# Kernel tuning notes

Measured on AMD Instinct MI355X. Metric: run time of the kernel, lower is better.

The kernel has to match this reference:

```python
import jax, jax.numpy as jnp
import numpy as np

D_MODEL = 1024
NUM_HEADS = 16
HEAD_DIM = D_MODEL // NUM_HEADS
B, T_Q, T_KV = 4, 4096, 4096


def setup_inputs() -> dict:
    key = jax.random.key(0)
    ks = jax.random.split(key, 10)
    s_in = 1.0 / np.sqrt(D_MODEL)
    s_out = 1.0 / np.sqrt(D_MODEL)
    return {
        "q": jax.random.normal(ks[0], (B, T_Q, D_MODEL), jnp.float32),
        "kv": jax.random.normal(ks[1], (B, T_KV, D_MODEL), jnp.float32),
        # per-head projection weights stacked: [H, d_model, head_dim]
        "Wq": jax.random.uniform(ks[2], (NUM_HEADS, D_MODEL, HEAD_DIM), jnp.float32, -s_in, s_in),
        "bq": jax.random.uniform(ks[3], (NUM_HEADS, HEAD_DIM), jnp.float32, -s_in, s_in),
        "Wk": jax.random.uniform(ks[4], (NUM_HEADS, D_MODEL, HEAD_DIM), jnp.float32, -s_in, s_in),
        "bk": jax.random.uniform(ks[5], (NUM_HEADS, HEAD_DIM), jnp.float32, -s_in, s_in),
        "Wv": jax.random.uniform(ks[6], (NUM_HEADS, D_MODEL, HEAD_DIM), jnp.float32, -s_in, s_in),
        "bv": jax.random.uniform(ks[7], (NUM_HEADS, HEAD_DIM), jnp.float32, -s_in, s_in),
        "Wo": jax.random.uniform(ks[8], (D_MODEL, D_MODEL), jnp.float32, -s_out, s_out),
        "bo": jax.random.uniform(ks[9], (D_MODEL,), jnp.float32, -s_out, s_out),
    }


def reference(q, kv, Wq, bq, Wk, bk, Wv, bv, Wo, bo):
    Bsz, Tq, _ = q.shape
    # per-head projections fused into one batched GEMM each: [b,t,d] x [h,d,e] -> [b,h,t,e]
    qh = jnp.einsum('btd,hde->bhte', q, Wq) + bq[None, :, None, :]
    kh = jnp.einsum('btd,hde->bhte', kv, Wk) + bk[None, :, None, :]
    vh = jnp.einsum('btd,hde->bhte', kv, Wv) + bv[None, :, None, :]
    # squared feature map
    qh = qh * qh
    kh = kh * kh
    # O(N) linear attention aggregation
    kv_sum = jnp.einsum('bhnd,bhne->bhde', kh, vh)           # [B,H,e,e]
    z = 1.0 / (jnp.einsum('bhnd,bhd->bhn', qh, kh.sum(axis=2)) + 1e-6)  # [B,H,Tq]
    attn = jnp.einsum('bhnd,bhde,bhn->bhne', qh, kv_sum, z)  # [B,H,Tq,e]
    attn = attn.transpose(0, 2, 1, 3).reshape(Bsz, Tq, D_MODEL)
    return attn @ Wo.T + bo
```

## Files before the change

kernel.cpp:

```cpp
#include <hip/hip_runtime.h>

#define BSZ 4
#define TSEQ 4096
#define DM 1024
#define NH 16
#define HD 64
#define BT (BSZ * TSEQ)
#define INV_LOSCALE (1.0f / 4096.0f)

using f32x4 = __attribute__((ext_vector_type(4))) float;
using f16x8 = __attribute__((ext_vector_type(8))) _Float16;
using u32x2 = __attribute__((ext_vector_type(2))) unsigned;
using u32x4 = __attribute__((ext_vector_type(4))) unsigned;

typedef const __attribute__((address_space(1))) void* gas_ptr;
typedef __attribute__((address_space(3))) void* las_ptr;

__device__ __forceinline__ void gload16(const void* g, void* l) {
    __builtin_amdgcn_global_load_lds((gas_ptr)g, (las_ptr)l, 16, 0, 0);
}

__device__ __forceinline__ void split1(float x, _Float16& h, _Float16& l) {
    h = (_Float16)x;
    l = (_Float16)((x - (float)h) * 4096.0f);
}
__device__ __forceinline__ unsigned pack2(_Float16 a, _Float16 b) {
    return (unsigned)__builtin_bit_cast(unsigned short, a) |
           ((unsigned)__builtin_bit_cast(unsigned short, b) << 16);
}
__device__ __forceinline__ f32x4 mfma_f16(f16x8 a, f16x8 b, f32x4 c) {
    return __builtin_amdgcn_mfma_f32_16x16x32_f16(a, b, c, 0, 0, 0);
}

__global__ __launch_bounds__(256) void fragsplit_kernel(const float* __restrict__ in,
        _Float16* __restrict__ hi, _Float16* __restrict__ lo) {
    const int C = blockIdx.x * 256 + threadIdx.x;
    const int l15 = C & 15, quad = (C >> 4) & 3, rb = (C >> 6) & 3;
    const int s = (C >> 8) & 31, panel = C >> 13;
    const size_t src = ((size_t)(panel * 64 + rb * 16 + l15)) * DM + s * 32 + quad * 8;
    f32x4 v0 = *(const f32x4*)&in[src];
    f32x4 v1 = *(const f32x4*)&in[src + 4];
    _Float16 h[8], l[8];
    #pragma unroll
    for (int j = 0; j < 4; ++j) { split1(v0[j], h[j], l[j]); split1(v1[j], h[4 + j], l[4 + j]); }
    ((u32x4*)hi)[C] = (u32x4){pack2(h[0],h[1]), pack2(h[2],h[3]), pack2(h[4],h[5]), pack2(h[6],h[7])};
    ((u32x4*)lo)[C] = (u32x4){pack2(l[0],l[1]), pack2(l[2],l[3]), pack2(l[4],l[5]), pack2(l[6],l[7])};
}

__global__ __launch_bounds__(256) void wsplit_kernel(
    const float* __restrict__ Wq, const float* __restrict__ Wk, const float* __restrict__ Wv,
    _Float16* __restrict__ qh, _Float16* __restrict__ ql,
    _Float16* __restrict__ kh, _Float16* __restrict__ kl,
    _Float16* __restrict__ vh, _Float16* __restrict__ vl) {
    const int tid = threadIdx.x;
    const int k0 = blockIdx.x * 64, h = blockIdx.y, w = blockIdx.z;
    const float* __restrict__ W = (w == 0) ? Wq : (w == 1) ? Wk : Wv;
    _Float16* __restrict__ dh = (w == 0) ? qh : (w == 1) ? kh : vh;
    _Float16* __restrict__ dl = (w == 0) ? ql : (w == 1) ? kl : vl;
    __shared__ __align__(16) float ws_[64][68];
    #pragma unroll
    for (int it = 0; it < 4; ++it) {
        int idx = it * 256 + tid;
        int r = idx >> 4, c4 = (idx & 15) * 4;
        *(f32x4*)&ws_[r][c4] = *(const f32x4*)&W[((size_t)h * DM + k0 + r) * HD + c4];
    }
    __syncthreads();
    const int n = tid >> 2, kq16 = (tid & 3) * 16;
    _Float16 hh[16], ll[16];
    #pragma unroll
    for (int j = 0; j < 16; ++j) split1(ws_[kq16 + j][n], hh[j], ll[j]);
    #pragma unroll
    for (int c = 0; c < 2; ++c) {
        int kg = k0 + kq16 + c * 8;
        int s = kg >> 5, quad = (kg >> 3) & 3;
        size_t chunk = (size_t)(h * 32 + s) * 256 + ((n >> 4) * 4 + quad) * 16 + (n & 15);
        ((u32x4*)dh)[chunk] = (u32x4){pack2(hh[c*8+0],hh[c*8+1]), pack2(hh[c*8+2],hh[c*8+3]),
                                      pack2(hh[c*8+4],hh[c*8+5]), pack2(hh[c*8+6],hh[c*8+7])};
        ((u32x4*)dl)[chunk] = (u32x4){pack2(ll[c*8+0],ll[c*8+1]), pack2(ll[c*8+2],ll[c*8+3]),
                                      pack2(ll[c*8+4],ll[c*8+5]), pack2(ll[c*8+6],ll[c*8+7])};
    }
}

__global__ __launch_bounds__(256, 2) void kv_stats_kernel(
    const _Float16* __restrict__ kv_hi, const _Float16* __restrict__ kv_lo,
    const _Float16* __restrict__ wkt_hi, const _Float16* __restrict__ wkt_lo,
    const _Float16* __restrict__ wvt_hi, const _Float16* __restrict__ wvt_lo,
    const float* __restrict__ bk, const float* __restrict__ bv,
    float* __restrict__ kv_sum, float* __restrict__ ksum)
{
    const int tid = threadIdx.x;
    const int lane = tid & 63, wave = tid >> 6, quad = lane >> 4, l15 = lane & 15;
    const int b = blockIdx.z, h = blockIdx.y, bx = blockIdx.x;

    __shared__ __align__(16) char smem[65536];
    float* khs = (float*)smem;
    float* vhs = (float*)(smem + 32768);

    const int isV = wave >> 1, half = wave & 1;
    const size_t btile = (size_t)h * 32;
    const int ty = tid >> 4, tx = tid & 15;

    f32x4 akv[4] = {};
    float aks[4] = {0.f, 0.f, 0.f, 0.f};

    for (int sub = 0; sub < 2; ++sub) {
        const size_t apan = (size_t)(b * 64 + bx * 4 + sub * 2);
        auto stage = [&](int p, int s) {
            char* dst = smem + p * 32768 + tid * 16;
            const size_t a0 = (apan * 32 + s) * 2048 + tid * 8;
            const size_t a1 = ((apan + 1) * 32 + s) * 2048 + tid * 8;
            const size_t bo = (btile + s) * 2048 + tid * 8;
            gload16(&kv_hi[a0], dst);
            gload16(&kv_hi[a1], dst + 4096);
            gload16(&kv_lo[a0], dst + 8192);
            gload16(&kv_lo[a1], dst + 12288);
            gload16(&wkt_hi[bo], dst + 16384);
            gload16(&wkt_lo[bo], dst + 20480);
            gload16(&wvt_hi[bo], dst + 24576);
            gload16(&wvt_lo[bo], dst + 28672);
        };

        f32x4 acc_h[4][4] = {}, acc_c[4][4] = {};
        stage(0, 0);
        for (int s = 0; s < 32; ++s) {
            const int p = s & 1;
            if (s < 31) {
                stage(p ^ 1, s + 1);
                asm volatile("s_waitcnt vmcnt(8)" ::: "memory");
            } else {
                asm volatile("s_waitcnt vmcnt(0)" ::: "memory");
            }
            __builtin_amdgcn_s_barrier();
            __builtin_amdgcn_sched_barrier(0);
            const char* bufc = smem + p * 32768;
            const _Float16* a_hi = (const _Float16*)bufc;
            const _Float16* a_lo = (const _Float16*)(bufc + 8192);
            const _Float16* bh = (const _Float16*)(bufc + (isV ? 24576 : 16384));
            const _Float16* bl = (const _Float16*)(bufc + (isV ? 28672 : 20480));
            f16x8 afh[4], afl[4], bfh[4], bfl[4];
            #pragma unroll
            for (int mt = 0; mt < 4; ++mt) {
                afh[mt] = *(const f16x8*)&a_hi[half * 2048 + mt * 512 + lane * 8];
                afl[mt] = *(const f16x8*)&a_lo[half * 2048 + mt * 512 + lane * 8];
            }
            #pragma unroll
            for (int nt = 0; nt < 4; ++nt) {
                bfh[nt] = *(const f16x8*)&bh[nt * 512 + lane * 8];
                bfl[nt] = *(const f16x8*)&bl[nt * 512 + lane * 8];
            }
            #pragma unroll
            for (int mt = 0; mt < 4; ++mt)
                #pragma unroll
                for (int nt = 0; nt < 4; ++nt) {
                    acc_h[mt][nt] = mfma_f16(afh[mt], bfh[nt], acc_h[mt][nt]);
                    acc_c[mt][nt] = mfma_f16(afh[mt], bfl[nt], acc_c[mt][nt]);
                    acc_c[mt][nt] = mfma_f16(afl[mt], bfh[nt], acc_c[mt][nt]);
                }
            __builtin_amdgcn_s_barrier();
            __builtin_amdgcn_sched_barrier(0);
        }

        {
            const float* __restrict__ bias = (isV ? bv : bk) + h * HD;
            float* __restrict__ outs = isV ? vhs : khs;
            float bia[4];
            #pragma unroll
            for (int nt = 0; nt < 4; ++nt) bia[nt] = bias[nt * 16 + l15];
            #pragma unroll
            for (int mt = 0; mt < 4; ++mt)
                #pragma unroll
                for (int nt = 0; nt < 4; ++nt)
                    #pragma unroll
                    for (int r = 0; r < 4; ++r) {
                        int t = half * 64 + mt * 16 + quad * 4 + r;
                        float v = acc_h[mt][nt][r] + INV_LOSCALE * acc_c[mt][nt][r] + bia[nt];
                        if (!isV) v = v * v;
                        outs[t * 64 + nt * 16 + l15] = v;
                    }
        }
        __syncthreads();

        #pragma unroll 4
        for (int t = 0; t < 128; ++t) {
            f32x4 kd = *(const f32x4*)&khs[t * 64 + ty * 4];
            f32x4 ve = *(const f32x4*)&vhs[t * 64 + tx * 4];
            #pragma unroll
            for (int i = 0; i < 4; ++i) {
                aks[i] += kd[i];
                akv[i] += kd[i] * ve;
            }
        }
        __syncthreads();
    }

    float* kvp = kv_sum + (size_t)(b * NH + h) * HD * HD;
    #pragma unroll
    for (int i = 0; i < 4; ++i)
        #pragma unroll
        for (int j = 0; j < 4; ++j)
            atomicAdd(&kvp[(ty * 4 + i) * HD + tx * 4 + j], akv[i][j]);
    if (tx == 0) {
        float* ksp = ksum + (b * NH + h) * HD;
        #pragma unroll
        for (int i = 0; i < 4; ++i) atomicAdd(&ksp[ty * 4 + i], aks[i]);
    }
}

__global__ __launch_bounds__(256, 3) void q_attn_ps_kernel(
    const _Float16* __restrict__ qf_hi, const _Float16* __restrict__ qf_lo,
    const _Float16* __restrict__ wqt_hi, const _Float16* __restrict__ wqt_lo,
    const float* __restrict__ bq,
    const float* __restrict__ kv_sum, const float* __restrict__ ksum,
    _Float16* __restrict__ attn_hi, _Float16* __restrict__ attn_lo)
{
    const int tid = threadIdx.x;
    const int lane = tid & 63, wave = tid >> 6, quad = lane >> 4, l15 = lane & 15;
    const int b = blockIdx.z, h = blockIdx.y, bx = blockIdx.x;

    __shared__ __align__(16) char smem[51200];
    __shared__ float z_s[128], ks_s[64];

    if (tid < 64) ks_s[tid] = ksum[(b * NH + h) * HD + tid];

    const size_t apan = (size_t)(b * 64 + bx * 2);
    const size_t btile = (size_t)h * 32;

    auto stage = [&](int p, int s) {
        char* dst = smem + p * 24576 + tid * 16;
        const size_t a0 = (apan * 32 + s) * 2048 + tid * 8;
        const size_t a1 = ((apan + 1) * 32 + s) * 2048 + tid * 8;
        const size_t bo = (btile + s) * 2048 + tid * 8;
        gload16(&qf_hi[a0], dst);
        gload16(&qf_hi[a1], dst + 4096);
        gload16(&qf_lo[a0], dst + 8192);
        gload16(&qf_lo[a1], dst + 12288);
        gload16(&wqt_hi[bo], dst + 16384);
        gload16(&wqt_lo[bo], dst + 20480);
    };

    f32x4 acc_h[2][4] = {}, acc_c[2][4] = {};
    stage(0, 0);
    for (int s = 0; s < 32; ++s) {
        const int p = s & 1;
        if (s < 31) {
            stage(p ^ 1, s + 1);
            asm volatile("s_waitcnt vmcnt(6)" ::: "memory");
        } else {
            asm volatile("s_waitcnt vmcnt(0)" ::: "memory");
        }
        __builtin_amdgcn_s_barrier();
        __builtin_amdgcn_sched_barrier(0);
        const char* bufc = smem + p * 24576;
        const _Float16* a_hi = (const _Float16*)bufc;
        const _Float16* a_lo = (const _Float16*)(bufc + 8192);
        f16x8 afh[2], afl[2], bfh[4], bfl[4];
        #pragma unroll
        for (int mt = 0; mt < 2; ++mt) {
            int fo = (wave * 2 + mt) * 512 + lane * 8;
            afh[mt] = *(const f16x8*)&a_hi[fo];
            afl[mt] = *(const f16x8*)&a_lo[fo];
        }
        #pragma unroll
        for (int nt = 0; nt < 4; ++nt) {
            bfh[nt] = *(const f16x8*)((const _Float16*)(bufc + 16384) + nt * 512 + lane * 8);
            bfl[nt] = *(const f16x8*)((const _Float16*)(bufc + 20480) + nt * 512 + lane * 8);
        }
        #pragma unroll
        for (int mt = 0; mt < 2; ++mt)
            #pragma unroll
            for (int nt = 0; nt < 4; ++nt) {
                acc_h[mt][nt] = mfma_f16(afh[mt], bfh[nt], acc_h[mt][nt]);
                acc_c[mt][nt] = mfma_f16(afh[mt], bfl[nt], acc_c[mt][nt]);
                acc_c[mt][nt] = mfma_f16(afl[mt], bfh[nt], acc_c[mt][nt]);
            }
        __builtin_amdgcn_s_barrier();
        __builtin_amdgcn_sched_barrier(0);
    }

    float* qs = (float*)smem;
    {
        const float* __restrict__ bias = bq + h * HD;
        float zp[2][4] = {};
        #pragma unroll
        for (int nt = 0; nt < 4; ++nt) {
            int d = nt * 16 + l15;
            float bia = bias[d];
            float ks  = ks_s[d];
            #pragma unroll
            for (int mt = 0; mt < 2; ++mt)
                #pragma unroll
                for (int r = 0; r < 4; ++r) {
                    int t = wave * 32 + mt * 16 + quad * 4 + r;
                    float v = acc_h[mt][nt][r] + INV_LOSCALE * acc_c[mt][nt][r] + bia;
                    float v2 = v * v;
                    qs[t * 68 + d] = v2;
                    zp[mt][r] = fmaf(v2, ks, zp[mt][r]);
                }
        }
        #pragma unroll
        for (int mt = 0; mt < 2; ++mt)
            #pragma unroll
            for (int r = 0; r < 4; ++r) {
                float p = zp[mt][r];
                p += __shfl_xor(p, 1);
                p += __shfl_xor(p, 2);
                p += __shfl_xor(p, 4);
                p += __shfl_xor(p, 8);
                if (l15 == 0) z_s[wave * 32 + mt * 16 + quad * 4 + r] = 1.f / (p + 1e-6f);
            }
    }
    __syncthreads();

    float* kvs = (float*)(smem + 34816);
    {
        const float* __restrict__ kvp = kv_sum + (size_t)(b * NH + h) * HD * HD;
        #pragma unroll
        for (int it = 0; it < 4; ++it) {
            int idx = it * 256 + tid;
            int r = idx >> 4, c = (idx & 15) * 4;
            *(f32x4*)&kvs[r * 64 + c] = *(const f32x4*)&kvp[r * HD + c];
        }
    }
    __syncthreads();

    const int ty = tid >> 4, tx = tid & 15;
    f32x4 sv[8] = {};
    #pragma unroll 4
    for (int d = 0; d < 64; d += 4) {
        f32x4 b0 = *(const f32x4*)&kvs[(d + 0) * 64 + tx * 4];
        f32x4 b1 = *(const f32x4*)&kvs[(d + 1) * 64 + tx * 4];
        f32x4 b2 = *(const f32x4*)&kvs[(d + 2) * 64 + tx * 4];
        f32x4 b3 = *(const f32x4*)&kvs[(d + 3) * 64 + tx * 4];
        #pragma unroll
        for (int i = 0; i < 8; ++i) {
            f32x4 av = *(const f32x4*)&qs[(ty * 8 + i) * 68 + d];
            sv[i] += av.x * b0 + av.y * b1 + av.z * b2 + av.w * b3;
        }
    }
    const int s_out = h * 2 + (tx >> 3);
    const int kq = (tx >> 1) & 3;
    const int rem8 = (tx & 1) * 8;
    #pragma unroll
    for (int i = 0; i < 8; ++i) {
        int t = ty * 8 + i;
        const size_t opanel = (size_t)b * 64 + bx * 2 + (t >> 6);
        const int tt = t & 63;
        f32x4 o = sv[i] * z_s[t];
        _Float16 hh[4], ll[4];
        #pragma unroll
        for (int j = 0; j < 4; ++j) split1(o[j], hh[j], ll[j]);
        size_t cb = (((opanel * 32 + s_out) * 256 + ((tt >> 4) * 4 + kq) * 16 + (tt & 15)) << 4) + rem8;
        *(u32x2*)((char*)attn_hi + cb) = (u32x2){pack2(hh[0], hh[1]), pack2(hh[2], hh[3])};
        *(u32x2*)((char*)attn_lo + cb) = (u32x2){pack2(ll[0], ll[1]), pack2(ll[2], ll[3])};
    }
}

__global__ __launch_bounds__(256, 3) void q_attn_kernel(
    const float* __restrict__ q,
    const _Float16* __restrict__ wqt_hi, const _Float16* __restrict__ wqt_lo,
    const float* __restrict__ bq,
    const float* __restrict__ kv_sum, const float* __restrict__ ksum,
    _Float16* __restrict__ attn_hi, _Float16* __restrict__ attn_lo)
{
    const int tid = threadIdx.x;
    const int lane = tid & 63, wave = tid >> 6, quad = lane >> 4, l15 = lane & 15;
    const int b = blockIdx.z, h = blockIdx.y, bx = blockIdx.x;
    const int t0 = bx * 64;

    __shared__ __align__(16) char smem[32768];
    __shared__ __align__(16) float qs[64 * 68];
    __shared__ float z_s[64], ks_s[64];

    if (tid < 64) ks_s[tid] = ksum[(b * NH + h) * HD + tid];

    const int arb = tid >> 6, aquad = (tid >> 4) & 3, al15 = tid & 15;
    const float* __restrict__ qrow =
        q + ((size_t)b * TSEQ + t0 + arb * 16 + al15) * DM + aquad * 8;
    const size_t btile = (size_t)h * 32;

    auto asplit_write = [&](int p, f32x4 v0, f32x4 v1) {
        _Float16 hh[8], ll[8];
        #pragma unroll
        for (int j = 0; j < 4; ++j) { split1(v0[j], hh[j], ll[j]); split1(v1[j], hh[4+j], ll[4+j]); }
        char* dst = smem + p * 16384 + tid * 16;
        *(u32x4*)dst =
            (u32x4){pack2(hh[0],hh[1]), pack2(hh[2],hh[3]), pack2(hh[4],hh[5]), pack2(hh[6],hh[7])};
        *(u32x4*)(dst + 4096) =
            (u32x4){pack2(ll[0],ll[1]), pack2(ll[2],ll[3]), pack2(ll[4],ll[5]), pack2(ll[6],ll[7])};
    };
    auto stageB = [&](int p, int s) {
        char* dst = smem + p * 16384 + 8192 + tid * 16;
        const size_t bo = (btile + s) * 2048 + tid * 8;
        gload16(&wqt_hi[bo], dst);
        gload16(&wqt_lo[bo], dst + 4096);
    };

    f32x4 acc_h[4] = {}, acc_c[4] = {};
    f32x4 v0 = *(const f32x4*)&qrow[0];
    f32x4 v1 = *(const f32x4*)&qrow[4];
    asplit_write(0, v0, v1);
    stageB(0, 0);
    v0 = *(const f32x4*)&qrow[32];
    v1 = *(const f32x4*)&qrow[36];
    asm volatile("s_waitcnt vmcnt(2) lgkmcnt(0)" ::: "memory");
    __builtin_amdgcn_s_barrier();
    __builtin_amdgcn_sched_barrier(0);

    for (int s = 0; s < 32; ++s) {
        const int p = s & 1;
        if (s < 31) {
            stageB(p ^ 1, s + 1);
            asplit_write(p ^ 1, v0, v1);
            if (s < 30) {
                v0 = *(const f32x4*)&qrow[(s + 2) * 32];
                v1 = *(const f32x4*)&qrow[(s + 2) * 32 + 4];
            }
            asm volatile("s_waitcnt vmcnt(4) lgkmcnt(0)" ::: "memory");
        } else {
            asm volatile("s_waitcnt vmcnt(0)" ::: "memory");
        }
        __builtin_amdgcn_s_barrier();
        __builtin_amdgcn_sched_barrier(0);
        const char* bufc = smem + p * 16384;
        f16x8 afh = *(const f16x8*)((const _Float16*)bufc + wave * 512 + lane * 8);
        f16x8 afl = *(const f16x8*)((const _Float16*)(bufc + 4096) + wave * 512 + lane * 8);
        f16x8 bfh[4], bfl[4];
        #pragma unroll
        for (int nt = 0; nt < 4; ++nt) {
            bfh[nt] = *(const f16x8*)((const _Float16*)(bufc + 8192) + nt * 512 + lane * 8);
            bfl[nt] = *(const f16x8*)((const _Float16*)(bufc + 12288) + nt * 512 + lane * 8);
        }
        #pragma unroll
        for (int nt = 0; nt < 4; ++nt) {
            acc_h[nt] = mfma_f16(afh, bfh[nt], acc_h[nt]);
            acc_c[nt] = mfma_f16(afh, bfl[nt], acc_c[nt]);
            acc_c[nt] = mfma_f16(afl, bfh[nt], acc_c[nt]);
        }
        __builtin_amdgcn_s_barrier();
        __builtin_amdgcn_sched_barrier(0);
    }

    {
        const int mrow0 = wave * 16;
        const float* __restrict__ bias = bq + h * HD;
        float zp[4] = {0.f, 0.f, 0.f, 0.f};
        #pragma unroll
        for (int nt = 0; nt < 4; ++nt) {
            int d = nt * 16 + l15;
            float bia = bias[d];
            float ks  = ks_s[d];
            #pragma unroll
            for (int r = 0; r < 4; ++r) {
                int t = mrow0 + quad * 4 + r;
                float v = acc_h[nt][r] + INV_LOSCALE * acc_c[nt][r] + bia;
                float v2 = v * v;
                qs[t * 68 + d] = v2;
                zp[r] = fmaf(v2, ks, zp[r]);
            }
        }
        #pragma unroll
        for (int r = 0; r < 4; ++r) {
            float p = zp[r];
            p += __shfl_xor(p, 1);
            p += __shfl_xor(p, 2);
            p += __shfl_xor(p, 4);
            p += __shfl_xor(p, 8);
            if (l15 == 0) z_s[mrow0 + quad * 4 + r] = 1.f / (p + 1e-6f);
        }
    }
    __syncthreads();

    float* kvs = (float*)smem;
    {
        const float* __restrict__ kvp = kv_sum + (size_t)(b * NH + h) * HD * HD;
        #pragma unroll
        for (int it = 0; it < 4; ++it) {
            int idx = it * 256 + tid;
            int r = idx >> 4, c = (idx & 15) * 4;
            *(f32x4*)&kvs[r * 64 + c] = *(const f32x4*)&kvp[r * HD + c];
        }
    }
    __syncthreads();

    const int ty = tid >> 4, tx = tid & 15;
    f32x4 sv[4] = {};
    #pragma unroll 4
    for (int d = 0; d < 64; d += 4) {
        f32x4 b0 = *(const f32x4*)&kvs[(d + 0) * 64 + tx * 4];
        f32x4 b1 = *(const f32x4*)&kvs[(d + 1) * 64 + tx * 4];
        f32x4 b2 = *(const f32x4*)&kvs[(d + 2) * 64 + tx * 4];
        f32x4 b3 = *(const f32x4*)&kvs[(d + 3) * 64 + tx * 4];
        #pragma unroll
        for (int i = 0; i < 4; ++i) {
            f32x4 av = *(const f32x4*)&qs[(ty * 4 + i) * 68 + d];
            sv[i] += av.x * b0 + av.y * b1 + av.z * b2 + av.w * b3;
        }
    }
    const size_t opanel = (size_t)b * 64 + bx;
    const int s_out = h * 2 + (tx >> 3);
    const int kq = (tx >> 1) & 3;
    const int rem8 = (tx & 1) * 8;
    #pragma unroll
    for (int i = 0; i < 4; ++i) {
        int t = ty * 4 + i;
        f32x4 o = sv[i] * z_s[t];
        _Float16 hh[4], ll[4];
        #pragma unroll
        for (int j = 0; j < 4; ++j) split1(o[j], hh[j], ll[j]);
        size_t cb = (((opanel * 32 + s_out) * 256 + ((t >> 4) * 4 + kq) * 16 + (t & 15)) << 4) + rem8;
        *(u32x2*)((char*)attn_hi + cb) = (u32x2){pack2(hh[0], hh[1]), pack2(hh[2], hh[3])};
        *(u32x2*)((char*)attn_lo + cb) = (u32x2){pack2(ll[0], ll[1]), pack2(ll[2], ll[3])};
    }
}

__global__ __launch_bounds__(256, 3) void out_proj_kernel(
    const _Float16* __restrict__ attn_hi, const _Float16* __restrict__ attn_lo,
    const _Float16* __restrict__ wo_hi, const _Float16* __restrict__ wo_lo,
    const float* __restrict__ bo, float* __restrict__ out)
{
    const int tid = threadIdx.x;
    const int lane = tid & 63, wave = tid >> 6, quad = lane >> 4, l15 = lane & 15;
    const int n0 = blockIdx.x * 64;
    const size_t m0 = (size_t)blockIdx.y * 128;

    __shared__ __align__(16) char smem[49152];
    float* cs = (float*)smem;

    const size_t ap0 = (m0 >> 6) * 32, ap1 = ap0 + 32;
    const size_t bpn = (size_t)(n0 >> 6) * 32;

    auto stage = [&](int p, int s) {
        char* dst = smem + p * 24576 + tid * 16;
        const size_t co = (size_t)s * 2048 + tid * 8;
        gload16(&attn_hi[ap0 * 2048 + co], dst);
        gload16(&attn_hi[ap1 * 2048 + co], dst + 4096);
        gload16(&attn_lo[ap0 * 2048 + co], dst + 8192);
        gload16(&attn_lo[ap1 * 2048 + co], dst + 12288);
        gload16(&wo_hi[bpn * 2048 + co],  dst + 16384);
        gload16(&wo_lo[bpn * 2048 + co],  dst + 20480);
    };

    const int panel = wave >> 1;
    f32x4 acc_h[2][4] = {}, acc_c[2][4] = {};
    stage(0, 0);
    for (int s = 0; s < 32; ++s) {
        const int p = s & 1;
        if (s < 31) {
            stage(p ^ 1, s + 1);
            asm volatile("s_waitcnt vmcnt(6)" ::: "memory");
        } else {
            asm volatile("s_waitcnt vmcnt(0)" ::: "memory");
        }
        __builtin_amdgcn_s_barrier();
        __builtin_amdgcn_sched_barrier(0);
        const char* bufc = smem + p * 24576;
        f16x8 afh[2], afl[2], bfh[4], bfl[4];
        #pragma unroll
        for (int mt = 0; mt < 2; ++mt) {
            int rbl = (wave & 1) * 2 + mt;
            afh[mt] = *(const f16x8*)((const _Float16*)(bufc + panel * 4096) + rbl * 512 + lane * 8);
            afl[mt] = *(const f16x8*)((const _Float16*)(bufc + 8192 + panel * 4096) + rbl * 512 + lane * 8);
        }
        #pragma unroll
        for (int nt = 0; nt < 4; ++nt) {
            bfh[nt] = *(const f16x8*)((const _Float16*)(bufc + 16384) + nt * 512 + lane * 8);
            bfl[nt] = *(const f16x8*)((const _Float16*)(bufc + 20480) + nt * 512 + lane * 8);
        }
        #pragma unroll
        for (int mt = 0; mt < 2; ++mt)
            #pragma unroll
            for (int nt = 0; nt < 4; ++nt) {
                acc_h[mt][nt] = mfma_f16(afh[mt], bfh[nt], acc_h[mt][nt]);
                acc_c[mt][nt] = mfma_f16(afh[mt], bfl[nt], acc_c[mt][nt]);
                acc_c[mt][nt] = mfma_f16(afl[mt], bfh[nt], acc_c[mt][nt]);
            }
        __builtin_amdgcn_s_barrier();
        __builtin_amdgcn_sched_barrier(0);
    }

    {
        float bia[4];
        #pragma unroll
        for (int nt = 0; nt < 4; ++nt) bia[nt] = bo[n0 + nt * 16 + l15];
        #pragma unroll
        for (int mt = 0; mt < 2; ++mt)
            #pragma unroll
            for (int nt = 0; nt < 4; ++nt)
                #pragma unroll
                for (int r = 0; r < 4; ++r) {
                    int t = wave * 32 + mt * 16 + quad * 4 + r;
                    cs[t * 64 + nt * 16 + l15] =
                        acc_h[mt][nt][r] + INV_LOSCALE * acc_c[mt][nt][r] + bia[nt];
                }
    }
    __syncthreads();
    #pragma unroll
    for (int it = 0; it < 8; ++it) {
        int idx = it * 256 + tid;
        int r = idx >> 4, c = (idx & 15) * 4;
        *(f32x4*)&out[(m0 + r) * DM + n0 + c] = *(f32x4*)&cs[r * 64 + c];
    }
}

extern "C" void kernel_launch(void* const* d_in, const int* in_sizes, int n_in,
                              void* d_out, int out_size, void* d_ws, size_t ws_size,
                              hipStream_t stream) {
    const float* q  = (const float*)d_in[0];
    const float* kv = (const float*)d_in[1];
    const float* Wq = (const float*)d_in[2];
    const float* bq = (const float*)d_in[3];
    const float* Wk = (const float*)d_in[4];
    const float* bk = (const float*)d_in[5];
    const float* Wv = (const float*)d_in[6];
    const float* bv = (const float*)d_in[7];
    const float* Wo = (const float*)d_in[8];
    const float* bo = (const float*)d_in[9];
    float* out = (float*)d_out;

    char* p = (char*)d_ws;
    float* kv_sum = (float*)p;              p += (size_t)BSZ * NH * HD * HD * 4;
    float* ksum   = (float*)p;              p += (size_t)BSZ * NH * HD * 4;
    _Float16* wqt_hi = (_Float16*)p;        p += (size_t)NH * HD * DM * 2;
    _Float16* wqt_lo = (_Float16*)p;        p += (size_t)NH * HD * DM * 2;
    _Float16* wkt_hi = (_Float16*)p;        p += (size_t)NH * HD * DM * 2;
    _Float16* wkt_lo = (_Float16*)p;        p += (size_t)NH * HD * DM * 2;
    _Float16* wvt_hi = (_Float16*)p;        p += (size_t)NH * HD * DM * 2;
    _Float16* wvt_lo = (_Float16*)p;        p += (size_t)NH * HD * DM * 2;
    _Float16* wo_hi  = (_Float16*)p;        p += (size_t)DM * DM * 2;
    _Float16* wo_lo  = (_Float16*)p;        p += (size_t)DM * DM * 2;
    _Float16* buf_hi = (_Float16*)p;        p += (size_t)BT * DM * 2;
    _Float16* buf_lo = (_Float16*)p;        p += (size_t)BT * DM * 2;
    _Float16* qf_hi  = (_Float16*)p;        p += (size_t)BT * DM * 2;
    _Float16* qf_lo  = (_Float16*)p;        p += (size_t)BT * DM * 2;
    const bool big = ws_size >= (size_t)(p - (char*)d_ws);

    size_t zero_bytes = ((size_t)BSZ * NH * HD * HD + (size_t)BSZ * NH * HD) * sizeof(float);
    hipMemsetAsync(d_ws, 0, zero_bytes, stream);

    fragsplit_kernel<<<(BT * DM / 8) / 256, 256, 0, stream>>>(kv, buf_hi, buf_lo);
    wsplit_kernel<<<dim3(DM / 64, NH, 3), 256, 0, stream>>>(
        Wq, Wk, Wv, wqt_hi, wqt_lo, wkt_hi, wkt_lo, wvt_hi, wvt_lo);
    fragsplit_kernel<<<(DM * DM / 8) / 256, 256, 0, stream>>>(Wo, wo_hi, wo_lo);

    kv_stats_kernel<<<dim3(TSEQ / 256, NH, BSZ), 256, 0, stream>>>(
        buf_hi, buf_lo, wkt_hi, wkt_lo, wvt_hi, wvt_lo, bk, bv, kv_sum, ksum);

    if (big) {
        fragsplit_kernel<<<(BT * DM / 8) / 256, 256, 0, stream>>>(q, qf_hi, qf_lo);
        q_attn_ps_kernel<<<dim3(TSEQ / 128, NH, BSZ), 256, 0, stream>>>(
            qf_hi, qf_lo, wqt_hi, wqt_lo, bq, kv_sum, ksum, buf_hi, buf_lo);
    } else {
        q_attn_kernel<<<dim3(TSEQ / 64, NH, BSZ), 256, 0, stream>>>(
            q, wqt_hi, wqt_lo, bq, kv_sum, ksum, buf_hi, buf_lo);
    }
    out_proj_kernel<<<dim3(DM / 64, BT / 128), 256, 0, stream>>>(
        buf_hi, buf_lo, wo_hi, wo_lo, bo, out);
}
```

Measured before the change: 650.5 us.

## Fold kv_sum into Wo per batch and use MFMA for KV statistics

Measured after the change: 626.0 us. 3.8% less time.

```diff
diff --git a/kernel.cpp b/kernel.cpp
--- a/kernel.cpp
+++ b/kernel.cpp
@@ -93,15 +93,18 @@
     const int b = blockIdx.z, h = blockIdx.y, bx = blockIdx.x;
 
     __shared__ __align__(16) char smem[65536];
-    float* khs = (float*)smem;
-    float* vhs = (float*)(smem + 32768);
+    _Float16* khT_h = (_Float16*)smem;
+    _Float16* khT_l = (_Float16*)(smem + 16384);
+    _Float16* vhT_h = (_Float16*)(smem + 32768);
+    _Float16* vhT_l = (_Float16*)(smem + 49152);
 
     const int isV = wave >> 1, half = wave & 1;
     const size_t btile = (size_t)h * 32;
-    const int ty = tid >> 4, tx = tid & 15;
-
-    f32x4 akv[4] = {};
-    float aks[4] = {0.f, 0.f, 0.f, 0.f};
+
+    f32x4 racc_h[4] = {}, racc_c[4] = {};
+    f32x4 rk_h = {}, rk_c = {};
+    const f16x8 ones = __builtin_bit_cast(f16x8,
+        (u32x4){0x3C003C00u, 0x3C003C00u, 0x3C003C00u, 0x3C003C00u});
 
     for (int sub = 0; sub < 2; ++sub) {
         const size_t apan = (size_t)(b * 64 + bx * 4 + sub * 2);
@@ -162,32 +165,46 @@
 
         {
             const float* __restrict__ bias = (isV ? bv : bk) + h * HD;
-            float* __restrict__ outs = isV ? vhs : khs;
+            _Float16* __restrict__ dh = isV ? vhT_h : khT_h;
+            _Float16* __restrict__ dl = isV ? vhT_l : khT_l;
             float bia[4];
             #pragma unroll
             for (int nt = 0; nt < 4; ++nt) bia[nt] = bias[nt * 16 + l15];
             #pragma unroll
-            for (int mt = 0; mt < 4; ++mt)
+            for (int mt = 0; mt < 4; ++mt) {
+                const int S = half * 2 + (mt >> 1);
+                const int tq = (mt & 1) * 2 + (quad >> 1);
+                const int eo = (quad & 1) * 4;
                 #pragma unroll
-                for (int nt = 0; nt < 4; ++nt)
+                for (int nt = 0; nt < 4; ++nt) {
+                    _Float16 hh[4], ll[4];
                     #pragma unroll
                     for (int r = 0; r < 4; ++r) {
-                        int t = half * 64 + mt * 16 + quad * 4 + r;
                         float v = acc_h[mt][nt][r] + INV_LOSCALE * acc_c[mt][nt][r] + bia[nt];
                         if (!isV) v = v * v;
-                        outs[t * 64 + nt * 16 + l15] = v;
+                        split1(v, hh[r], ll[r]);
                     }
+                    int fo = S * 2048 + (nt * 4 + tq) * 128 + l15 * 8 + eo;
+                    *(u32x2*)&dh[fo] = (u32x2){pack2(hh[0], hh[1]), pack2(hh[2], hh[3])};
+                    *(u32x2*)&dl[fo] = (u32x2){pack2(ll[0], ll[1]), pack2(ll[2], ll[3])};
+                }
+            }
         }
         __syncthreads();
 
-        #pragma unroll 4
-        for (int t = 0; t < 128; ++t) {
-            f32x4 kd = *(const f32x4*)&khs[t * 64 + ty * 4];
-            f32x4 ve = *(const f32x4*)&vhs[t * 64 + tx * 4];
-            #pragma unroll
-            for (int i = 0; i < 4; ++i) {
-                aks[i] += kd[i];
-                akv[i] += kd[i] * ve;
+        #pragma unroll
+        for (int S = 0; S < 4; ++S) {
+            f16x8 ah = *(const f16x8*)&khT_h[S * 2048 + wave * 512 + lane * 8];
+            f16x8 al = *(const f16x8*)&khT_l[S * 2048 + wave * 512 + lane * 8];
+            rk_h = mfma_f16(ah, ones, rk_h);
+            rk_c = mfma_f16(al, ones, rk_c);
+            #pragma unroll
+            for (int nt = 0; nt < 4; ++nt) {
+                f16x8 bh = *(const f16x8*)&vhT_h[S * 2048 + nt * 512 + lane * 8];
+                f16x8 bl = *(const f16x8*)&vhT_l[S * 2048 + nt * 512 + lane * 8];
+                racc_h[nt] = mfma_f16(ah, bh, racc_h[nt]);
+                racc_c[nt] = mfma_f16(ah, bl, racc_c[nt]);
+                racc_c[nt] = mfma_f16(al, bh, racc_c[nt]);
             }
         }
         __syncthreads();
@@ -195,29 +212,76 @@
 
     float* kvp = kv_sum + (size_t)(b * NH + h) * HD * HD;
     #pragma unroll
-    for (int i = 0; i < 4; ++i)
-        #pragma unroll
-        for (int j = 0; j < 4; ++j)
-            atomicAdd(&kvp[(ty * 4 + i) * HD + tx * 4 + j], akv[i][j]);
-    if (tx == 0) {
+    for (int nt = 0; nt < 4; ++nt)
+        #pragma unroll
+        for (int r = 0; r < 4; ++r)
+            atomicAdd(&kvp[(wave * 16 + quad * 4 + r) * HD + nt * 16 + l15],
+                      racc_h[nt][r] + INV_LOSCALE * racc_c[nt][r]);
+    if (l15 == 0) {
         float* ksp = ksum + (b * NH + h) * HD;
         #pragma unroll
-        for (int i = 0; i < 4; ++i) atomicAdd(&ksp[ty * 4 + i], aks[i]);
+        for (int r = 0; r < 4; ++r)
+            atomicAdd(&ksp[wave * 16 + quad * 4 + r], rk_h[r] + INV_LOSCALE * rk_c[r]);
+    }
+}
+
+__global__ __launch_bounds__(256) void pmat_kernel(
+    const float* __restrict__ kv_sum, const float* __restrict__ Wo,
+    _Float16* __restrict__ pt_hi, _Float16* __restrict__ pt_lo)
+{
+    const int tid = threadIdx.x;
+    const int opan = blockIdx.x, h = blockIdx.y, b = blockIdx.z;
+    __shared__ __align__(16) float kvsT[64][68];
+    __shared__ __align__(16) float wos[64][68];
+    const float* __restrict__ kvp = kv_sum + (size_t)(b * NH + h) * HD * HD;
+    #pragma unroll
+    for (int it = 0; it < 4; ++it) {
+        int idx = it * 256 + tid;
+        int d = idx >> 4, e4 = (idx & 15) * 4;
+        f32x4 v = *(const f32x4*)&kvp[d * HD + e4];
+        kvsT[e4 + 0][d] = v.x; kvsT[e4 + 1][d] = v.y;
+        kvsT[e4 + 2][d] = v.z; kvsT[e4 + 3][d] = v.w;
+        int o = idx >> 4;
+        *(f32x4*)&wos[o][e4] = *(const f32x4*)&Wo[(size_t)(opan * 64 + o) * DM + h * HD + e4];
+    }
+    __syncthreads();
+    const int ty = tid >> 4, tx = tid & 15;
+    f32x4 sv[4] = {};
+    #pragma unroll 8
+    for (int e = 0; e < 64; ++e) {
+        f32x4 kv4 = *(const f32x4*)&kvsT[e][tx * 4];
+        #pragma unroll
+        for (int i = 0; i < 4; ++i) sv[i] += wos[ty * 4 + i][e] * kv4;
+    }
+    const int d0 = tx * 4;
+    const int S = h * 2 + (d0 >> 5);
+    const int kq = (d0 >> 3) & 3;
+    const int rem8 = (d0 & 4) ? 8 : 0;
+    #pragma unroll
+    for (int i = 0; i < 4; ++i) {
+        int ol = ty * 4 + i;
+        f32x4 o4 = sv[i] * INV_LOSCALE;
+        _Float16 hh[4], ll[4];
+        #pragma unroll
+        for (int j = 0; j < 4; ++j) split1(o4[j], hh[j], ll[j]);
+        size_t cb = ((((size_t)(b * 16 + opan) * 32 + S) * 256 +
+                      ((ol >> 4) * 4 + kq) * 16 + (ol & 15)) << 4) + rem8;
+        *(u32x2*)((char*)pt_hi + cb) = (u32x2){pack2(hh[0], hh[1]), pack2(hh[2], hh[3])};
+        *(u32x2*)((char*)pt_lo + cb) = (u32x2){pack2(ll[0], ll[1]), pack2(ll[2], ll[3])};
     }
 }
 
 __global__ __launch_bounds__(256, 3) void q_attn_ps_kernel(
     const _Float16* __restrict__ qf_hi, const _Float16* __restrict__ qf_lo,
     const _Float16* __restrict__ wqt_hi, const _Float16* __restrict__ wqt_lo,
-    const float* __restrict__ bq,
-    const float* __restrict__ kv_sum, const float* __restrict__ ksum,
+    const float* __restrict__ bq, const float* __restrict__ ksum,
     _Float16* __restrict__ attn_hi, _Float16* __restrict__ attn_lo)
 {
     const int tid = threadIdx.x;
     const int lane = tid & 63, wave = tid >> 6, quad = lane >> 4, l15 = lane & 15;
     const int b = blockIdx.z, h = blockIdx.y, bx = blockIdx.x;
 
-    __shared__ __align__(16) char smem[51200];
+    __shared__ __align__(16) char smem[49152];
     __shared__ float z_s[128], ks_s[64];
 
     if (tid < 64) ks_s[tid] = ksum[(b * NH + h) * HD + tid];
@@ -306,52 +370,31 @@
                 p += __shfl_xor(p, 2);
                 p += __shfl_xor(p, 4);
                 p += __shfl_xor(p, 8);
-                if (l15 == 0) z_s[wave * 32 + mt * 16 + quad * 4 + r] = 1.f / (p + 1e-6f);
+                if (l15 == 0) z_s[wave * 32 + mt * 16 + quad * 4 + r] = 4096.0f / (p + 1e-6f);
             }
     }
     __syncthreads();
 
-    float* kvs = (float*)(smem + 34816);
-    {
-        const float* __restrict__ kvp = kv_sum + (size_t)(b * NH + h) * HD * HD;
-        #pragma unroll
-        for (int it = 0; it < 4; ++it) {
-            int idx = it * 256 + tid;
-            int r = idx >> 4, c = (idx & 15) * 4;
-            *(f32x4*)&kvs[r * 64 + c] = *(const f32x4*)&kvp[r * HD + c];
-        }
-    }
-    __syncthreads();
-
-    const int ty = tid >> 4, tx = tid & 15;
-    f32x4 sv[8] = {};
-    #pragma unroll 4
-    for (int d = 0; d < 64; d += 4) {
-        f32x4 b0 = *(const f32x4*)&kvs[(d + 0) * 64 + tx * 4];
-        f32x4 b1 = *(const f32x4*)&kvs[(d + 1) * 64 + tx * 4];
-        f32x4 b2 = *(const f32x4*)&kvs[(d + 2) * 64 + tx * 4];
-        f32x4 b3 = *(const f32x4*)&kvs[(d + 3) * 64 + tx * 4];
-        #pragma unroll
-        for (int i = 0; i < 8; ++i) {
-            f32x4 av = *(const f32x4*)&qs[(ty * 8 + i) * 68 + d];
-            sv[i] += av.x * b0 + av.y * b1 + av.z * b2 + av.w * b3;
-        }
-    }
-    const int s_out = h * 2 + (tx >> 3);
-    const int kq = (tx >> 1) & 3;
-    const int rem8 = (tx & 1) * 8;
-    #pragma unroll
-    for (int i = 0; i < 8; ++i) {
-        int t = ty * 8 + i;
-        const size_t opanel = (size_t)b * 64 + bx * 2 + (t >> 6);
-        const int tt = t & 63;
-        f32x4 o = sv[i] * z_s[t];
-        _Float16 hh[4], ll[4];
-        #pragma unroll
-        for (int j = 0; j < 4; ++j) split1(o[j], hh[j], ll[j]);
-        size_t cb = (((opanel * 32 + s_out) * 256 + ((tt >> 4) * 4 + kq) * 16 + (tt & 15)) << 4) + rem8;
-        *(u32x2*)((char*)attn_hi + cb) = (u32x2){pack2(hh[0], hh[1]), pack2(hh[2], hh[3])};
-        *(u32x2*)((char*)attn_lo + cb) = (u32x2){pack2(ll[0], ll[1]), pack2(ll[2], ll[3])};
+    #pragma unroll
+    for (int it = 0; it < 4; ++it) {
+        int cid = it * 256 + tid;
+        int lp = cid >> 9, Sl = (cid >> 8) & 1, c = cid & 255;
+        int t = lp * 64 + (c >> 6) * 16 + (c & 15);
+        int d = Sl * 32 + ((c >> 4) & 3) * 8;
+        f32x4 a0 = *(const f32x4*)&qs[t * 68 + d];
+        f32x4 a1 = *(const f32x4*)&qs[t * 68 + d + 4];
+        float z = z_s[t];
+        _Float16 hh[8], ll[8];
+        #pragma unroll
+        for (int j = 0; j < 4; ++j) {
+            split1(z * a0[j], hh[j], ll[j]);
+            split1(z * a1[j], hh[4 + j], ll[4 + j]);
+        }
+        size_t cb = (((size_t)(b * 64 + bx * 2 + lp) * 32 + h * 2 + Sl) * 256 + c) << 4;
+        *(u32x4*)((char*)attn_hi + cb) =
+            (u32x4){pack2(hh[0],hh[1]), pack2(hh[2],hh[3]), pack2(hh[4],hh[5]), pack2(hh[6],hh[7])};
+        *(u32x4*)((char*)attn_lo + cb) =
+            (u32x4){pack2(ll[0],ll[1]), pack2(ll[2],ll[3]), pack2(ll[4],ll[5]), pack2(ll[6],ll[7])};
     }
 }
 
@@ -513,6 +556,98 @@
     }
 }
 
+__global__ __launch_bounds__(256, 3) void out_proj_p_kernel(
+    const _Float16* __restrict__ attn_hi, const _Float16* __restrict__ attn_lo,
+    const _Float16* __restrict__ pt_hi, const _Float16* __restrict__ pt_lo,
+    const float* __restrict__ bo, float* __restrict__ out)
+{
+    const int tid = threadIdx.x;
+    const int lane = tid & 63, wave = tid >> 6, quad = lane >> 4, l15 = lane & 15;
+    const int n0 = blockIdx.x * 64;
+    const size_t m0 = (size_t)blockIdx.y * 128;
+
+    __shared__ __align__(16) char smem[49152];
+    float* cs = (float*)smem;
+
+    const size_t ap0 = (m0 >> 6) * 32, ap1 = ap0 + 32;
+    const int bb = (int)(m0 >> 12);
+    const _Float16* __restrict__ pbh = pt_hi + (size_t)bb * 16 * 32 * 2048;
+    const _Float16* __restrict__ pbl = pt_lo + (size_t)bb * 16 * 32 * 2048;
+    const size_t bpn = (size_t)(n0 >> 6) * 32;
+
+    auto stage = [&](int p, int s) {
+        char* dst = smem + p * 24576 + tid * 16;
+        const size_t co = (size_t)s * 2048 + tid * 8;
+        gload16(&attn_hi[ap0 * 2048 + co], dst);
+        gload16(&attn_hi[ap1 * 2048 + co], dst + 4096);
+        gload16(&attn_lo[ap0 * 2048 + co], dst + 8192);
+        gload16(&attn_lo[ap1 * 2048 + co], dst + 12288);
+        gload16(&pbh[(bpn + s) * 2048 + tid * 8], dst + 16384);
+        gload16(&pbl[(bpn + s) * 2048 + tid * 8], dst + 20480);
+    };
+
+    const int panel = wave >> 1;
+    f32x4 acc_h[2][4] = {}, acc_c[2][4] = {};
+    stage(0, 0);
+    for (int s = 0; s < 32; ++s) {
+        const int p = s & 1;
+        if (s < 31) {
+            stage(p ^ 1, s + 1);
+            asm volatile("s_waitcnt vmcnt(6)" ::: "memory");
+        } else {
+            asm volatile("s_waitcnt vmcnt(0)" ::: "memory");
+        }
+        __builtin_amdgcn_s_barrier();
+        __builtin_amdgcn_sched_barrier(0);
+        const char* bufc = smem + p * 24576;
+        f16x8 afh[2], afl[2], bfh[4], bfl[4];
+        #pragma unroll
+        for (int mt = 0; mt < 2; ++mt) {
+            int rbl = (wave & 1) * 2 + mt;
+            afh[mt] = *(const f16x8*)((const _Float16*)(bufc + panel * 4096) + rbl * 512 + lane * 8);
+            afl[mt] = *(const f16x8*)((const _Float16*)(bufc + 8192 + panel * 4096) + rbl * 512 + lane * 8);
+        }
+        #pragma unroll
+        for (int nt = 0; nt < 4; ++nt) {
+            bfh[nt] = *(const f16x8*)((const _Float16*)(bufc + 16384) + nt * 512 + lane * 8);
+            bfl[nt] = *(const f16x8*)((const _Float16*)(bufc + 20480) + nt * 512 + lane * 8);
+        }
+        #pragma unroll
+        for (int mt = 0; mt < 2; ++mt)
+            #pragma unroll
+            for (int nt = 0; nt < 4; ++nt) {
+                acc_h[mt][nt] = mfma_f16(afh[mt], bfh[nt], acc_h[mt][nt]);
+                acc_c[mt][nt] = mfma_f16(afh[mt], bfl[nt], acc_c[mt][nt]);
+                acc_c[mt][nt] = mfma_f16(afl[mt], bfh[nt], acc_c[mt][nt]);
+            }
+        __builtin_amdgcn_s_barrier();
+        __builtin_amdgcn_sched_barrier(0);
+    }
+
+    {
+        float bia[4];
+        #pragma unroll
+        for (int nt = 0; nt < 4; ++nt) bia[nt] = bo[n0 + nt * 16 + l15];
+        #pragma unroll
+        for (int mt = 0; mt < 2; ++mt)
+            #pragma unroll
+            for (int nt = 0; nt < 4; ++nt)
+                #pragma unroll
+                for (int r = 0; r < 4; ++r) {
+                    int t = wave * 32 + mt * 16 + quad * 4 + r;
+                    cs[t * 64 + nt * 16 + l15] =
+                        acc_h[mt][nt][r] + INV_LOSCALE * acc_c[mt][nt][r] + bia[nt];
+                }
+    }
+    __syncthreads();
+    #pragma unroll
+    for (int it = 0; it < 8; ++it) {
+        int idx = it * 256 + tid;
+        int r = idx >> 4, c = (idx & 15) * 4;
+        *(f32x4*)&out[(m0 + r) * DM + n0 + c] = *(f32x4*)&cs[r * 64 + c];
+    }
+}
+
 __global__ __launch_bounds__(256, 3) void out_proj_kernel(
     const _Float16* __restrict__ attn_hi, const _Float16* __restrict__ attn_lo,
     const _Float16* __restrict__ wo_hi, const _Float16* __restrict__ wo_lo,
@@ -536,8 +671,8 @@
         gload16(&attn_hi[ap1 * 2048 + co], dst + 4096);
         gload16(&attn_lo[ap0 * 2048 + co], dst + 8192);
         gload16(&attn_lo[ap1 * 2048 + co], dst + 12288);
-        gload16(&wo_hi[bpn * 2048 + co],  dst + 16384);
-        gload16(&wo_lo[bpn * 2048 + co],  dst + 20480);
+        gload16(&wo_hi[(bpn + s) * 2048 + tid * 8], dst + 16384);
+        gload16(&wo_lo[(bpn + s) * 2048 + tid * 8], dst + 20480);
     };
 
     const int panel = wave >> 1;
@@ -632,6 +767,8 @@
     _Float16* buf_lo = (_Float16*)p;        p += (size_t)BT * DM * 2;
     _Float16* qf_hi  = (_Float16*)p;        p += (size_t)BT * DM * 2;
     _Float16* qf_lo  = (_Float16*)p;        p += (size_t)BT * DM * 2;
+    _Float16* pt_hi  = (_Float16*)p;        p += (size_t)BSZ * DM * DM * 2;
+    _Float16* pt_lo  = (_Float16*)p;        p += (size_t)BSZ * DM * DM * 2;
     const bool big = ws_size >= (size_t)(p - (char*)d_ws);
 
     size_t zero_bytes = ((size_t)BSZ * NH * HD * HD + (size_t)BSZ * NH * HD) * sizeof(float);
@@ -640,19 +777,23 @@
     fragsplit_kernel<<<(BT * DM / 8) / 256, 256, 0, stream>>>(kv, buf_hi, buf_lo);
     wsplit_kernel<<<dim3(DM / 64, NH, 3), 256, 0, stream>>>(
         Wq, Wk, Wv, wqt_hi, wqt_lo, wkt_hi, wkt_lo, wvt_hi, wvt_lo);
-    fragsplit_kernel<<<(DM * DM / 8) / 256, 256, 0, stream>>>(Wo, wo_hi, wo_lo);
+    if (!big)
+        fragsplit_kernel<<<(DM * DM / 8) / 256, 256, 0, stream>>>(Wo, wo_hi, wo_lo);
 
     kv_stats_kernel<<<dim3(TSEQ / 256, NH, BSZ), 256, 0, stream>>>(
         buf_hi, buf_lo, wkt_hi, wkt_lo, wvt_hi, wvt_lo, bk, bv, kv_sum, ksum);
 
     if (big) {
         fragsplit_kernel<<<(BT * DM / 8) / 256, 256, 0, stream>>>(q, qf_hi, qf_lo);
+        pmat_kernel<<<dim3(16, NH, BSZ), 256, 0, stream>>>(kv_sum, Wo, pt_hi, pt_lo);
         q_attn_ps_kernel<<<dim3(TSEQ / 128, NH, BSZ), 256, 0, stream>>>(
-            qf_hi, qf_lo, wqt_hi, wqt_lo, bq, kv_sum, ksum, buf_hi, buf_lo);
+            qf_hi, qf_lo, wqt_hi, wqt_lo, bq, ksum, buf_hi, buf_lo);
+        out_proj_p_kernel<<<dim3(DM / 64, BT / 128), 256, 0, stream>>>(
+            buf_hi, buf_lo, pt_hi, pt_lo, bo, out);
     } else {
         q_attn_kernel<<<dim3(TSEQ / 64, NH, BSZ), 256, 0, stream>>>(
             q, wqt_hi, wqt_lo, bq, kv_sum, ksum, buf_hi, buf_lo);
-    }
-    out_proj_kernel<<<dim3(DM / 64, BT / 128), 256, 0, stream>>>(
-        buf_hi, buf_lo, wo_hi, wo_lo, bo, out);
-}
+        out_proj_kernel<<<dim3(DM / 64, BT / 128), 256, 0, stream>>>(
+            buf_hi, buf_lo, wo_hi, wo_lo, bo, out);
+    }
+}
```
